# Performance work log

Hardware: AMD Instinct MI355X
Metric: run time of the kernel (lower is better)

## Reference

```python
import jax, jax.numpy as jnp
import numpy as np

B, N, C = 2, 2048, 1152
H = 16
HD = C // H  # 72
SCALE = HD ** -0.5
NEG = -100000000.0  # -1e8 bias for fp32 masked positions


def setup_inputs() -> dict:
    key = jax.random.key(0)
    k1, k2, k3, k4, k5 = jax.random.split(key, 5)
    x = jax.random.normal(k1, (B, N, C), dtype=jnp.float32)
    attn_mask = jax.random.randint(k2, (B, N), 0, 2, dtype=jnp.int32)
    w_qkv = jax.random.normal(k3, (3 * C, C), dtype=jnp.float32) * 0.02
    w_proj = jax.random.normal(k4, (C, C), dtype=jnp.float32) * 0.02
    b_proj = jax.random.normal(k5, (C,), dtype=jnp.float32) * 0.02
    return {"x": x, "attn_mask": attn_mask, "w_qkv": w_qkv, "w_proj": w_proj, "b_proj": b_proj}


def reference(x, attn_mask, w_qkv, w_proj, b_proj):
    # qkv projection: [B,N,3C] -> [3,B,H,N,HD]
    qkv = (x @ w_qkv.T).reshape(B, N, 3, H, HD).transpose(2, 0, 3, 1, 4)
    q, k, v = qkv[0], qkv[1], qkv[2]

    # additive mask bias from outer product of per-token 0/1 mask
    m = attn_mask.astype(x.dtype)          # [B,N]
    mm = m[:, :, None] * m[:, None, :]      # [B,N,N]
    bias = jnp.where(mm == 0, NEG, jnp.where(mm == 1, 0.0, mm))
    bias = bias[:, None, :, :]              # [B,1,N,N] broadcast over heads

    # math-branch attention: full QK^T, bias add, softmax, NaN patch, AV
    attn = jnp.einsum('bhqd,bhkd->bhqk', q, k) * SCALE + bias
    attn = jax.nn.softmax(attn, axis=-1)
    attn = jnp.where(jnp.isnan(attn), 0.0, attn)
    out = jnp.einsum('bhqk,bhkd->bqhd', attn, v).reshape(B, N, C)

    return out @ w_proj.T + b_proj
```

## Files before the change

kernel.cpp:

```cpp
#include <hip/hip_runtime.h>

#define B_   2
#define N_   2048
#define C_   1152
#define H_   16
#define HD_  72
#define QKV_W 3456
#define SCALE_ 0.11785113019775793f
#define NEG_  -100000000.0f
#define HDP  96
#define HDV  80
#define PRE_  0.1700219068852255f
#define FMAX_ 4.0f
#define KNEG_ 16384.0f

typedef __bf16    bf16x8 __attribute__((ext_vector_type(8)));
typedef _Float16  f16x8  __attribute__((ext_vector_type(8)));
typedef _Float16  f16x4  __attribute__((ext_vector_type(4)));
typedef float     f32x4  __attribute__((ext_vector_type(4)));

#define GLOAD_LDS16(gp, lp)                                                    \
  __builtin_amdgcn_global_load_lds(                                            \
      (const __attribute__((address_space(1))) void*)(gp),                     \
      (__attribute__((address_space(3))) void*)(lp), 16, 0, 0)

static __device__ __forceinline__ unsigned pack2h(_Float16 a, _Float16 b) {
  union { _Float16 h[2]; unsigned u; } u;
  u.h[0] = a; u.h[1] = b; return u.u;
}

__global__ __launch_bounds__(256)
void split3_f16(const float* __restrict__ x, const float* __restrict__ wq,
                const float* __restrict__ wp,
                _Float16* __restrict__ xf, _Float16* __restrict__ wqf,
                _Float16* __restrict__ wpf,
                float* __restrict__ meanAcc, int nmv,
                int n8x, int n8q, int n8p) {
  int i = blockIdx.x * 256 + threadIdx.x;
  if (i < nmv) meanAcc[i] = 0.0f;
  const float* src; _Float16* dst;
  if (i < n8x) { src = x; dst = xf; }
  else if (i < n8x + n8q) { i -= n8x; src = wq; dst = wqf; }
  else {
    i -= n8x + n8q;
    if (i >= n8p) return;
    src = wp; dst = wpf;
  }
  const float4* p = (const float4*)src + (size_t)i * 2;
  float4 a = p[0], b = p[1];
  float xs[8] = {a.x, a.y, a.z, a.w, b.x, b.y, b.z, b.w};
  f16x8 hv;
#pragma unroll
  for (int r = 0; r < 8; ++r) hv[r] = (_Float16)xs[r];
  *(f16x8*)(dst + (size_t)i * 8) = hv;
}

__global__ __launch_bounds__(256)
void gemm_f16(const _Float16* __restrict__ A, const _Float16* __restrict__ Bm,
              const float* __restrict__ bias, float* __restrict__ Cout,
              int M, int Nn, int K) {
  __shared__ uint4 lds[2][1024];

  const int tid  = threadIdx.x;
  const int wv   = tid >> 6;
  const int lane = tid & 63;
  const int wm   = wv >> 1;
  const int wn   = wv & 1;
  const int m0 = blockIdx.x * 128, n0 = blockIdx.y * 128;

  const char* gp[4];
  int gd[4];
#pragma unroll
  for (int i = 0; i < 4; ++i) {
    const int gid = wv * 4 + i;
    if (gid < 8) {
      gd[i] = gid * 64;
      gp[i] = (const char*)(A + (size_t)(m0 + gid * 16 + (lane & 15)) * K +
                            ((lane >> 4) << 3));
    } else {
      const int g2 = gid - 8;
      gd[i] = 512 + g2 * 64;
      gp[i] = (const char*)(Bm + (size_t)(n0 + g2 * 16 + (lane & 15)) * K +
                            ((lane >> 4) << 3));
    }
  }

#pragma unroll
  for (int i = 0; i < 4; ++i) {
    GLOAD_LDS16(gp[i], &lds[0][gd[i]]);
    gp[i] += 64;
  }

  f32x4 acc[4][4] = {};
  const int nk = K >> 5;

  for (int kt = 0; kt < nk; ++kt) {
    const int cur = kt & 1, nxt = cur ^ 1;
    __syncthreads();

    if (kt < nk - 1) {
#pragma unroll
      for (int i = 0; i < 4; ++i) {
        GLOAD_LDS16(gp[i], &lds[nxt][gd[i]]);
        gp[i] += 64;
      }
    }

    const uint4* cbuf = lds[cur];
    f16x8 af[4], bf[4];
#pragma unroll
    for (int t = 0; t < 4; ++t) {
      af[t] = *(const f16x8*)&cbuf[(wm * 4 + t) * 64 + lane];
      bf[t] = *(const f16x8*)&cbuf[512 + (wn * 4 + t) * 64 + lane];
    }
#pragma unroll
    for (int i = 0; i < 4; ++i)
#pragma unroll
      for (int j = 0; j < 4; ++j)
        acc[i][j] = __builtin_amdgcn_mfma_f32_16x16x32_f16(af[i], bf[j], acc[i][j], 0, 0, 0);
  }

  const int cl = lane & 15, rq = (lane >> 4) << 2;
#pragma unroll
  for (int j = 0; j < 4; ++j) {
    const int col = n0 + (wn * 4 + j) * 16 + cl;
    const float bv = bias ? bias[col] : 0.0f;
#pragma unroll
    for (int i = 0; i < 4; ++i) {
      const int row = m0 + (wm * 4 + i) * 16 + rq;
#pragma unroll
      for (int r = 0; r < 4; ++r)
        Cout[(size_t)(row + r) * Nn + col] = acc[i][j][r] + bv;
    }
  }
}

__global__ __launch_bounds__(256)
void prep_qkv(const float* __restrict__ qkv, const int* __restrict__ mask,
              _Float16* __restrict__ Qf, _Float16* __restrict__ Kf,
              _Float16* __restrict__ Vt, float* __restrict__ meanAcc) {
  const int nt = blockIdx.x, h = blockIdx.y, b = blockIdx.z;
  const int n0 = nt * 64, bh = b * H_ + h, tid = threadIdx.x;
  __shared__ float vls[64][73];

#pragma unroll
  for (int s = 0; s < 2; ++s) {
    const float* src = qkv + (size_t)(b * N_ + n0) * QKV_W + s * C_ + h * HD_;
    _Float16* of = (s == 0 ? Qf : Kf) + ((size_t)bh * N_ + n0) * HDP;
    for (int idx = tid; idx < 64 * 18; idx += 256) {
      const int row = idx / 18, c = idx % 18, d0 = c * 4;
      float4 v = *(const float4*)(src + (size_t)row * QKV_W + d0);
      if (s == 0) { v.x *= PRE_; v.y *= PRE_; v.z *= PRE_; v.w *= PRE_; }
      f16x4 hv;
      hv[0] = (_Float16)v.x; hv[1] = (_Float16)v.y;
      hv[2] = (_Float16)v.z; hv[3] = (_Float16)v.w;
      *(f16x4*)(of + (size_t)row * HDP + d0) = hv;
    }
  }

  for (int idx = tid; idx < 64 * 3; idx += 256) {
    const int row = idx / 3, c3 = idx % 3;
    const int n = n0 + row;
    f16x8 z = {};
    f16x8 qp = z, kp = z;
    if (c3 == 0) {
      qp[0] = (_Float16)1.0f;
      const int kb = (mask[b * N_ + n] != 0);
      kp[0] = (_Float16)(kb ? -FMAX_ : -KNEG_);
    }
    const size_t base = ((size_t)bh * N_ + n) * HDP + 72 + c3 * 8;
    *(f16x8*)(Qf + base) = qp;
    *(f16x8*)(Kf + base) = kp;
  }

  const float* vsrc = qkv + (size_t)(b * N_ + n0) * QKV_W + 2 * C_ + h * HD_;
  for (int idx = tid; idx < 64 * 18; idx += 256) {
    const int row = idx / 18, c = idx % 18, d0 = c * 4;
    float4 v = *(const float4*)(vsrc + (size_t)row * QKV_W + d0);
    vls[row][d0] = v.x; vls[row][d0 + 1] = v.y;
    vls[row][d0 + 2] = v.z; vls[row][d0 + 3] = v.w;
  }
  __syncthreads();
  if (tid < HD_) {
    float sum = 0.0f;
#pragma unroll 8
    for (int r = 0; r < 64; ++r) sum += vls[r][tid];
    atomicAdd(&meanAcc[bh * HD_ + tid], sum);
  }
  for (int idx = tid; idx < HDV * 64; idx += 256) {
    const int d = idx >> 6, nn = idx & 63;
    const float v = (d < HD_) ? vls[nn][d] : 0.0f;
    Vt[((size_t)bh * HDV + d) * N_ + n0 + nn] = (_Float16)v;
  }
}

__global__ __launch_bounds__(256)
void attn_mfma(const _Float16* __restrict__ Qf, const _Float16* __restrict__ Kf,
               const _Float16* __restrict__ Vt, const float* __restrict__ meanV,
               const int* __restrict__ mask, _Float16* __restrict__ att) {
  const int bh = blockIdx.x, qt = blockIdx.y;
  const int b = bh >> 4, h = bh & 15;
  const int tid = threadIdx.x, wv = tid >> 6, lane = tid & 63;
  const int lq = lane & 15;
  const int lg = lane >> 4;
  const int q0 = qt * 128;

  __shared__ uint4 lds[2][22 * 64];
  __shared__ __align__(16) _Float16 Pbuf[2][4][16][72];

  f16x8 qh[2][3];
#pragma unroll
  for (int bd = 0; bd < 2; ++bd) {
    const size_t qoff =
        ((size_t)bh * N_ + q0 + bd * 64 + wv * 16 + lq) * HDP + lg * 8;
#pragma unroll
    for (int c = 0; c < 3; ++c)
      qh[bd][c] = *(const f16x8*)(Qf + qoff + c * 32);
  }

  const _Float16* kb = Kf + (size_t)bh * N_ * HDP;
  const _Float16* vb = Vt + (size_t)bh * HDV * (size_t)N_;

  const int gstart = (wv < 2) ? wv * 6 : 12 + (wv - 2) * 5;
  const int gcount = (wv < 2) ? 6 : 5;
  const char* gptr[6];
  long gstepB[6];
  int gdst[6];
#pragma unroll
  for (int i = 0; i < 6; ++i) {
    int gid = gstart + i;
    if (gid > 21) gid = 21;
    gdst[i] = gid * 64;
    if (gid < 12) {
      const int tile = gid / 3, ch = gid - tile * 3;
      gptr[i] = (const char*)(kb + (size_t)(tile * 16 + lq) * HDP + ch * 32 + lg * 8);
      gstepB[i] = 64 * HDP * 2;
    } else {
      const int v = gid - 12, td = v >> 1, ck = v & 1;
      gptr[i] = (const char*)(vb + (size_t)(td * 16 + lq) * N_ + ck * 32 + lg * 8);
      gstepB[i] = 64 * 2;
    }
  }

#pragma unroll
  for (int i = 0; i < 6; ++i)
    if (i < gcount) {
      GLOAD_LDS16(gptr[i], &lds[0][gdst[i]]);
      gptr[i] += gstepB[i];
    }

  float l_run[2] = {0.0f, 0.0f};
  f32x4 Oacc[2][5] = {};

  for (int kt = 0; kt < N_ / 64; ++kt) {
    const int cur = kt & 1, nxt = cur ^ 1;
    __syncthreads();

    if (kt < N_ / 64 - 1) {
#pragma unroll
      for (int i = 0; i < 6; ++i)
        if (i < gcount) {
          GLOAD_LDS16(gptr[i], &lds[nxt][gdst[i]]);
          gptr[i] += gstepB[i];
        }
    }

    const uint4* cbuf = lds[cur];

    f32x4 s[2][4] = {};
#pragma unroll
    for (int ch = 0; ch < 3; ++ch)
#pragma unroll
      for (int t = 0; t < 4; ++t) {
        f16x8 kf = *(const f16x8*)&cbuf[(t * 3 + ch) * 64 + lane];
        s[0][t] = __builtin_amdgcn_mfma_f32_16x16x32_f16(kf, qh[0][ch], s[0][t], 0, 0, 0);
        s[1][t] = __builtin_amdgcn_mfma_f32_16x16x32_f16(kf, qh[1][ch], s[1][t], 0, 0, 0);
      }

#pragma unroll
    for (int bd = 0; bd < 2; ++bd) {
      float psum = 0.0f;
#pragma unroll
      for (int t = 0; t < 4; ++t) {
        const float p0 = exp2f(s[bd][t][0]);
        const float p1 = exp2f(s[bd][t][1]);
        const float p2 = exp2f(s[bd][t][2]);
        const float p3 = exp2f(s[bd][t][3]);
        psum += (p0 + p1) + (p2 + p3);
        *(uint2*)&Pbuf[bd][wv][lq][t * 16 + 4 * lg] =
            make_uint2(pack2h((_Float16)p0, (_Float16)p1),
                       pack2h((_Float16)p2, (_Float16)p3));
      }
      l_run[bd] += psum;
    }

#pragma unroll
    for (int ck = 0; ck < 2; ++ck) {
      f16x8 pf0 = *(const f16x8*)&Pbuf[0][wv][lq][ck * 32 + lg * 8];
      f16x8 pf1 = *(const f16x8*)&Pbuf[1][wv][lq][ck * 32 + lg * 8];
#pragma unroll
      for (int td = 0; td < 5; ++td) {
        f16x8 vf = *(const f16x8*)&cbuf[(12 + td * 2 + ck) * 64 + lane];
        Oacc[0][td] = __builtin_amdgcn_mfma_f32_16x16x32_f16(vf, pf0, Oacc[0][td], 0, 0, 0);
        Oacc[1][td] = __builtin_amdgcn_mfma_f32_16x16x32_f16(vf, pf1, Oacc[1][td], 0, 0, 0);
      }
    }
  }

  __syncthreads();
  float* osc = (float*)lds;
  float* myo = osc + wv * 16 * 81;
  const int rq = lane >> 2, jj = lane & 3;

#pragma unroll
  for (int bd = 0; bd < 2; ++bd) {
    float l = l_run[bd];
    l += __shfl_xor(l, 16);
    l += __shfl_xor(l, 32);
    const float inv = 1.0f / l;
#pragma unroll
    for (int td = 0; td < 5; ++td)
#pragma unroll
      for (int r = 0; r < 4; ++r)
        myo[lq * 81 + td * 16 + 4 * lg + r] = Oacc[bd][td][r] * inv;
    __syncthreads();

    const int q = q0 + bd * 64 + wv * 16 + rq;
    const int qm = (mask[b * N_ + q] != 0);
    const float* rowp = myo + rq * 81 + jj * 18;
    const float* mvp  = meanV + bh * HD_ + jj * 18;
    const size_t obase = ((size_t)(b * N_) + q) * C_ + h * HD_ + jj * 18;
#pragma unroll
    for (int e = 0; e < 9; ++e) {
      const float a = qm ? rowp[2 * e]     : mvp[2 * e]     * (1.0f / 2048.0f);
      const float c = qm ? rowp[2 * e + 1] : mvp[2 * e + 1] * (1.0f / 2048.0f);
      *(unsigned*)(att + obase + 2 * e) = pack2h((_Float16)a, (_Float16)c);
    }
    __syncthreads();
  }
}

__global__ __launch_bounds__(256)
void gemm64_nt(const float* __restrict__ A, const float* __restrict__ Bm,
               const float* __restrict__ bias, float* __restrict__ C,
               int M, int N, int K) {
  __shared__ __align__(16) float As[32][68];
  __shared__ __align__(16) float Bs[32][68];
  const int tid = threadIdx.x;
  const int tx = tid & 15, ty = tid >> 4;
  const int m0 = blockIdx.x * 64, n0 = blockIdx.y * 64;
  float acc[4][4] = {};
  for (int k0 = 0; k0 < K; k0 += 32) {
#pragma unroll
    for (int i = 0; i < 2; ++i) {
      const int idx = tid + i * 256;
      const int row = idx >> 3, kc = (idx & 7) << 2;
      float4 a = *(const float4*)(A + (size_t)(m0 + row) * K + k0 + kc);
      As[kc + 0][row] = a.x; As[kc + 1][row] = a.y;
      As[kc + 2][row] = a.z; As[kc + 3][row] = a.w;
      float4 b = *(const float4*)(Bm + (size_t)(n0 + row) * K + k0 + kc);
      Bs[kc + 0][row] = b.x; Bs[kc + 1][row] = b.y;
      Bs[kc + 2][row] = b.z; Bs[kc + 3][row] = b.w;
    }
    __syncthreads();
#pragma unroll
    for (int k = 0; k < 32; ++k) {
      float4 av4 = *(const float4*)&As[k][ty << 2];
      float4 bv4 = *(const float4*)&Bs[k][tx << 2];
      float av[4] = {av4.x, av4.y, av4.z, av4.w};
      float bv[4] = {bv4.x, bv4.y, bv4.z, bv4.w};
#pragma unroll
      for (int i = 0; i < 4; ++i)
#pragma unroll
        for (int j = 0; j < 4; ++j) acc[i][j] += av[i] * bv[j];
    }
    __syncthreads();
  }
#pragma unroll
  for (int i = 0; i < 4; ++i) {
    const int row = m0 + (ty << 2) + i, col = n0 + (tx << 2);
    float4 v = make_float4(acc[i][0], acc[i][1], acc[i][2], acc[i][3]);
    if (bias) {
      v.x += bias[col + 0]; v.y += bias[col + 1];
      v.z += bias[col + 2]; v.w += bias[col + 3];
    }
    *(float4*)(C + (size_t)row * N + col) = v;
  }
}

__global__ __launch_bounds__(256)
void attn_kernel(const float* __restrict__ qkv, const int* __restrict__ mask,
                 float* __restrict__ out) {
  const int qt = blockIdx.x, h = blockIdx.y, b = blockIdx.z;
  const int tid = threadIdx.x;
  const int q0 = qt * 64;
  __shared__ __align__(16) float qT[HD_][68];
  __shared__ __align__(16) float kT[HD_][68];
  __shared__ __align__(16) float vT[HD_][68];
  __shared__ float rowm[64], rowl[64], rowa[64];
  __shared__ float biask[64];
  __shared__ int   mq[64];
  float (*ps)[68] = (float (*)[68])kT;
  const float* qg = qkv + (size_t)(b * N_ + q0) * QKV_W + h * HD_;
  for (int idx = tid; idx < 64 * HD_; idx += 256) {
    const int qi = idx / HD_, d = idx % HD_;
    qT[d][qi] = qg[(size_t)qi * QKV_W + d];
  }
  if (tid < 64) {
    rowm[tid] = -1e30f; rowl[tid] = 0.0f;
    mq[tid] = mask[b * N_ + q0 + tid];
  }
  const int sqg = tid >> 4, skg = tid & 15;
  const int oqg = tid >> 3, ods = tid & 7;
  float o[4][9];
#pragma unroll
  for (int i = 0; i < 4; ++i)
#pragma unroll
    for (int dd = 0; dd < 9; ++dd) o[i][dd] = 0.0f;
  __syncthreads();
  for (int kt = 0; kt < N_ / 64; ++kt) {
    const int k0 = kt * 64;
    const float* kg = qkv + (size_t)(b * N_ + k0) * QKV_W + C_ + h * HD_;
    const float* vg = qkv + (size_t)(b * N_ + k0) * QKV_W + 2 * C_ + h * HD_;
    for (int idx = tid; idx < 64 * HD_; idx += 256) {
      const int kj = idx / HD_, d = idx % HD_;
      kT[d][kj] = kg[(size_t)kj * QKV_W + d];
      vT[d][kj] = vg[(size_t)kj * QKV_W + d];
    }
    if (tid < 64) biask[tid] = (mask[b * N_ + k0 + tid] != 0) ? 0.0f : NEG_;
    __syncthreads();
    float sacc[4][4] = {};
    for (int d = 0; d < HD_; ++d) {
      float4 qv4 = *(const float4*)&qT[d][sqg << 2];
      float4 kv4 = *(const float4*)&kT[d][skg << 2];
      float qa[4] = {qv4.x, qv4.y, qv4.z, qv4.w};
      float ka[4] = {kv4.x, kv4.y, kv4.z, kv4.w};
#pragma unroll
      for (int i = 0; i < 4; ++i)
#pragma unroll
        for (int j = 0; j < 4; ++j) sacc[i][j] += qa[i] * ka[j];
    }
    __syncthreads();
#pragma unroll
    for (int i = 0; i < 4; ++i) {
      const int qi = (sqg << 2) + i;
      const int qm2 = mq[qi];
#pragma unroll
      for (int j = 0; j < 4; ++j) {
        const int kj = (skg << 2) + j;
        const float bias = (qm2 != 0) ? biask[kj] : NEG_;
        ps[qi][kj] = sacc[i][j] * SCALE_ + bias;
      }
    }
    __syncthreads();
    if (tid < 64) {
      float mt = -1e30f;
#pragma unroll
      for (int j4 = 0; j4 < 16; ++j4) {
        float4 p4 = *(const float4*)&ps[tid][j4 << 2];
        mt = fmaxf(mt, fmaxf(fmaxf(p4.x, p4.y), fmaxf(p4.z, p4.w)));
      }
      const float mo = rowm[tid];
      const float nm = fmaxf(mo, mt);
      const float a = __expf(mo - nm);
      float sum = 0.0f;
#pragma unroll
      for (int j4 = 0; j4 < 16; ++j4) {
        float4 p4 = *(const float4*)&ps[tid][j4 << 2];
        p4.x = __expf(p4.x - nm); p4.y = __expf(p4.y - nm);
        p4.z = __expf(p4.z - nm); p4.w = __expf(p4.w - nm);
        sum += p4.x + p4.y + p4.z + p4.w;
        *(float4*)&ps[tid][j4 << 2] = p4;
      }
      rowl[tid] = rowl[tid] * a + sum;
      rowm[tid] = nm;
      rowa[tid] = a;
    }
    __syncthreads();
    if (tid < 128) {
#pragma unroll
      for (int i = 0; i < 4; ++i) {
        const float a = rowa[(oqg << 2) + i];
#pragma unroll
        for (int dd = 0; dd < 9; ++dd) o[i][dd] *= a;
      }
      for (int k4 = 0; k4 < 16; ++k4) {
        float4 pv4[4];
#pragma unroll
        for (int i = 0; i < 4; ++i)
          pv4[i] = *(const float4*)&ps[(oqg << 2) + i][k4 << 2];
        float pa[4][4];
#pragma unroll
        for (int i = 0; i < 4; ++i) {
          pa[i][0] = pv4[i].x; pa[i][1] = pv4[i].y;
          pa[i][2] = pv4[i].z; pa[i][3] = pv4[i].w;
        }
#pragma unroll
        for (int dd = 0; dd < 9; ++dd) {
          float4 vv4 = *(const float4*)&vT[ods * 9 + dd][k4 << 2];
          float va[4] = {vv4.x, vv4.y, vv4.z, vv4.w};
#pragma unroll
          for (int i = 0; i < 4; ++i)
            o[i][dd] += pa[i][0] * va[0] + pa[i][1] * va[1] +
                        pa[i][2] * va[2] + pa[i][3] * va[3];
        }
      }
    }
    __syncthreads();
  }
  if (tid < 128) {
#pragma unroll
    for (int i = 0; i < 4; ++i) {
      const int qi = (oqg << 2) + i;
      const float inv = 1.0f / rowl[qi];
      const size_t base = (size_t)(b * N_ + q0 + qi) * C_ + h * HD_ + ods * 9;
#pragma unroll
      for (int dd = 0; dd < 9; ++dd) out[base + dd] = o[i][dd] * inv;
    }
  }
}

extern "C" void kernel_launch(void* const* d_in, const int* in_sizes, int n_in,
                              void* d_out, int out_size, void* d_ws, size_t ws_size,
                              hipStream_t stream) {
  (void)in_sizes; (void)n_in; (void)out_size;

  const float* x      = (const float*)d_in[0];
  const int*   mask   = (const int*)  d_in[1];
  const float* w_qkv  = (const float*)d_in[2];
  const float* w_proj = (const float*)d_in[3];
  const float* b_proj = (const float*)d_in[4];
  float* out = (float*)d_out;

  const size_t XE = (size_t)B_ * N_ * C_;
  const size_t WQ = (size_t)QKV_W * C_;
  const size_t WP = (size_t)C_ * C_;
  const size_t QKVE = (size_t)B_ * N_ * QKV_W;
  const size_t QKE  = (size_t)B_ * H_ * N_ * HDP;
  const size_t VTE  = (size_t)B_ * H_ * HDV * N_;
  const int    MVN  = B_ * H_ * HD_;

  char* w = (char*)d_ws;
  float*    qkv = (float*)w;
  _Float16* att = (_Float16*)w;
  char* A0 = w + QKVE * 4;
  _Float16* x_f  = (_Float16*)A0;
  _Float16* wq_f = x_f + XE;
  _Float16* wp_f = wq_f + WQ;
  _Float16* Qf   = wp_f + WP;
  _Float16* Kf   = Qf + QKE;
  _Float16* Vt   = Kf + QKE;
  float* meanAcc = (float*)(Vt + VTE);
  const size_t need = (size_t)((char*)(meanAcc + MVN) - w);

  if (ws_size >= need) {
    const int n8x = (int)(XE / 8), n8q = (int)(WQ / 8), n8p = (int)(WP / 8);
    const int nblk = (n8x + n8q + n8p + 255) / 256;
    split3_f16<<<nblk, 256, 0, stream>>>(x, w_qkv, w_proj, x_f, wq_f, wp_f,
                                         meanAcc, MVN, n8x, n8q, n8p);

    gemm_f16<<<dim3(32, 27), 256, 0, stream>>>(x_f, wq_f, nullptr, qkv,
                                               B_ * N_, QKV_W, C_);
    prep_qkv<<<dim3(32, 16, 2), 256, 0, stream>>>(qkv, mask, Qf, Kf, Vt, meanAcc);

    attn_mfma<<<dim3(32, 16), 256, 0, stream>>>(Qf, Kf, Vt, meanAcc, mask, att);

    gemm_f16<<<dim3(32, 9), 256, 0, stream>>>(att, wp_f, b_proj, out,
                                              B_ * N_, C_, C_);
  } else {
    float* qkv_f = (float*)d_ws;
    float* att_f = qkv_f + QKVE;
    gemm64_nt<<<dim3(64, 54), 256, 0, stream>>>(x, w_qkv, nullptr, qkv_f,
                                                B_ * N_, QKV_W, C_);
    attn_kernel<<<dim3(32, 16, 2), 256, 0, stream>>>(qkv_f, mask, att_f);
    gemm64_nt<<<dim3(64, 18), 256, 0, stream>>>(att_f, w_proj, b_proj, out,
                                                B_ * N_, C_, C_);
  }
}
```

Baseline: 298.2 us.

## Fuse QKV layout prep into QKV GEMM epilogue, drop fp32 intermediate

Removes the prep_qkv kernel and the fp32 QKV intermediate buffer. The QKV GEMM epilogue now writes Q (pre-scaled), K, and transposed V directly in fp16, and accumulates per-head V column sums via shuffles and atomics. The padding columns and mask entries are written by the conversion kernel instead. This saves a kernel launch and an fp32 round trip through global memory. The cost is scattered 2-byte stores in the Q/K epilogue.

Result: faster. 281.3 us (-5.7%).

```diff
diff --git a/kernel.cpp b/kernel.cpp
--- a/kernel.cpp
+++ b/kernel.cpp
@@ -14,7 +14,6 @@
 #define FMAX_ 4.0f
 #define KNEG_ 16384.0f
 
-typedef __bf16    bf16x8 __attribute__((ext_vector_type(8)));
 typedef _Float16  f16x8  __attribute__((ext_vector_type(8)));
 typedef _Float16  f16x4  __attribute__((ext_vector_type(4)));
 typedef float     f32x4  __attribute__((ext_vector_type(4)));
@@ -34,18 +33,50 @@
                 const float* __restrict__ wp,
                 _Float16* __restrict__ xf, _Float16* __restrict__ wqf,
                 _Float16* __restrict__ wpf,
+                _Float16* __restrict__ Qf, _Float16* __restrict__ Kf,
+                _Float16* __restrict__ Vt, const int* __restrict__ mask,
                 float* __restrict__ meanAcc, int nmv,
                 int n8x, int n8q, int n8p) {
   int i = blockIdx.x * 256 + threadIdx.x;
   if (i < nmv) meanAcc[i] = 0.0f;
-  const float* src; _Float16* dst;
+
+  const float* src = nullptr; _Float16* dst = nullptr;
   if (i < n8x) { src = x; dst = xf; }
-  else if (i < n8x + n8q) { i -= n8x; src = wq; dst = wqf; }
   else {
-    i -= n8x + n8q;
-    if (i >= n8p) return;
-    src = wp; dst = wpf;
-  }
+    i -= n8x;
+    if (i < n8q) { src = wq; dst = wqf; }
+    else {
+      i -= n8q;
+      if (i < n8p) { src = wp; dst = wpf; }
+      else {
+        i -= n8p;
+        if (i < 32 * 2048 * 3) {
+          const int bh = i / (2048 * 3);
+          int rem = i - bh * (2048 * 3);
+          const int n = rem / 3, c3 = rem - (rem / 3) * 3;
+          f16x8 qp = {}, kp = {};
+          if (c3 == 0) {
+            qp[0] = (_Float16)1.0f;
+            const int kb = (mask[(bh >> 4) * N_ + n] != 0);
+            kp[0] = (_Float16)(kb ? -FMAX_ : -KNEG_);
+          }
+          const size_t base = ((size_t)bh * N_ + n) * HDP + 72 + c3 * 8;
+          *(f16x8*)(Qf + base) = qp;
+          *(f16x8*)(Kf + base) = kp;
+          return;
+        }
+        i -= 32 * 2048 * 3;
+        if (i < 32 * 8 * 256) {
+          const int bh = i >> 11, rem = i & 2047;
+          const int dp = rem >> 8, nc = rem & 255;
+          f16x8 z = {};
+          *(f16x8*)(Vt + ((size_t)bh * HDV + 72 + dp) * N_ + nc * 8) = z;
+        }
+        return;
+      }
+    }
+  }
+
   const float4* p = (const float4*)src + (size_t)i * 2;
   float4 a = p[0], b = p[1];
   float xs[8] = {a.x, a.y, a.z, a.w, b.x, b.y, b.z, b.w};
@@ -136,61 +167,116 @@
 }
 
 __global__ __launch_bounds__(256)
-void prep_qkv(const float* __restrict__ qkv, const int* __restrict__ mask,
-              _Float16* __restrict__ Qf, _Float16* __restrict__ Kf,
-              _Float16* __restrict__ Vt, float* __restrict__ meanAcc) {
-  const int nt = blockIdx.x, h = blockIdx.y, b = blockIdx.z;
-  const int n0 = nt * 64, bh = b * H_ + h, tid = threadIdx.x;
-  __shared__ float vls[64][73];
-
-#pragma unroll
-  for (int s = 0; s < 2; ++s) {
-    const float* src = qkv + (size_t)(b * N_ + n0) * QKV_W + s * C_ + h * HD_;
-    _Float16* of = (s == 0 ? Qf : Kf) + ((size_t)bh * N_ + n0) * HDP;
-    for (int idx = tid; idx < 64 * 18; idx += 256) {
-      const int row = idx / 18, c = idx % 18, d0 = c * 4;
-      float4 v = *(const float4*)(src + (size_t)row * QKV_W + d0);
-      if (s == 0) { v.x *= PRE_; v.y *= PRE_; v.z *= PRE_; v.w *= PRE_; }
-      f16x4 hv;
-      hv[0] = (_Float16)v.x; hv[1] = (_Float16)v.y;
-      hv[2] = (_Float16)v.z; hv[3] = (_Float16)v.w;
-      *(f16x4*)(of + (size_t)row * HDP + d0) = hv;
-    }
-  }
-
-  for (int idx = tid; idx < 64 * 3; idx += 256) {
-    const int row = idx / 3, c3 = idx % 3;
-    const int n = n0 + row;
-    f16x8 z = {};
-    f16x8 qp = z, kp = z;
-    if (c3 == 0) {
-      qp[0] = (_Float16)1.0f;
-      const int kb = (mask[b * N_ + n] != 0);
-      kp[0] = (_Float16)(kb ? -FMAX_ : -KNEG_);
-    }
-    const size_t base = ((size_t)bh * N_ + n) * HDP + 72 + c3 * 8;
-    *(f16x8*)(Qf + base) = qp;
-    *(f16x8*)(Kf + base) = kp;
-  }
-
-  const float* vsrc = qkv + (size_t)(b * N_ + n0) * QKV_W + 2 * C_ + h * HD_;
-  for (int idx = tid; idx < 64 * 18; idx += 256) {
-    const int row = idx / 18, c = idx % 18, d0 = c * 4;
-    float4 v = *(const float4*)(vsrc + (size_t)row * QKV_W + d0);
-    vls[row][d0] = v.x; vls[row][d0 + 1] = v.y;
-    vls[row][d0 + 2] = v.z; vls[row][d0 + 3] = v.w;
-  }
-  __syncthreads();
-  if (tid < HD_) {
-    float sum = 0.0f;
-#pragma unroll 8
-    for (int r = 0; r < 64; ++r) sum += vls[r][tid];
-    atomicAdd(&meanAcc[bh * HD_ + tid], sum);
-  }
-  for (int idx = tid; idx < HDV * 64; idx += 256) {
-    const int d = idx >> 6, nn = idx & 63;
-    const float v = (d < HD_) ? vls[nn][d] : 0.0f;
-    Vt[((size_t)bh * HDV + d) * N_ + n0 + nn] = (_Float16)v;
+void gemm_qkv_fused(const _Float16* __restrict__ A, const _Float16* __restrict__ Bm,
+                    _Float16* __restrict__ Qf, _Float16* __restrict__ Kf,
+                    _Float16* __restrict__ Vt, float* __restrict__ meanAcc) {
+  __shared__ uint4 lds[2][1024];
+
+  const int K = C_;
+  const int tid  = threadIdx.x;
+  const int wv   = tid >> 6;
+  const int lane = tid & 63;
+  const int wm   = wv >> 1;
+  const int wn   = wv & 1;
+  const int m0 = blockIdx.x * 128, n0 = blockIdx.y * 128;
+
+  const char* gp[4];
+  int gd[4];
+#pragma unroll
+  for (int i = 0; i < 4; ++i) {
+    const int gid = wv * 4 + i;
+    if (gid < 8) {
+      gd[i] = gid * 64;
+      gp[i] = (const char*)(A + (size_t)(m0 + gid * 16 + (lane & 15)) * K +
+                            ((lane >> 4) << 3));
+    } else {
+      const int g2 = gid - 8;
+      gd[i] = 512 + g2 * 64;
+      gp[i] = (const char*)(Bm + (size_t)(n0 + g2 * 16 + (lane & 15)) * K +
+                            ((lane >> 4) << 3));
+    }
+  }
+
+#pragma unroll
+  for (int i = 0; i < 4; ++i) {
+    GLOAD_LDS16(gp[i], &lds[0][gd[i]]);
+    gp[i] += 64;
+  }
+
+  f32x4 acc[4][4] = {};
+  const int nk = K >> 5;
+
+  for (int kt = 0; kt < nk; ++kt) {
+    const int cur = kt & 1, nxt = cur ^ 1;
+    __syncthreads();
+
+    if (kt < nk - 1) {
+#pragma unroll
+      for (int i = 0; i < 4; ++i) {
+        GLOAD_LDS16(gp[i], &lds[nxt][gd[i]]);
+        gp[i] += 64;
+      }
+    }
+
+    const uint4* cbuf = lds[cur];
+    f16x8 af[4], bf[4];
+#pragma unroll
+    for (int t = 0; t < 4; ++t) {
+      af[t] = *(const f16x8*)&cbuf[(wm * 4 + t) * 64 + lane];
+      bf[t] = *(const f16x8*)&cbuf[512 + (wn * 4 + t) * 64 + lane];
+    }
+#pragma unroll
+    for (int i = 0; i < 4; ++i)
+#pragma unroll
+      for (int j = 0; j < 4; ++j)
+        acc[i][j] = __builtin_amdgcn_mfma_f32_16x16x32_f16(af[i], bf[j], acc[i][j], 0, 0, 0);
+  }
+
+  const int s = n0 / C_;
+  const int b = m0 >> 11;
+  const int nloc = m0 & 2047;
+  const int cl = lane & 15, rq = (lane >> 4) << 2;
+
+  if (s < 2) {
+    _Float16* dst = (s == 0) ? Qf : Kf;
+    const float sc = (s == 0) ? PRE_ : 1.0f;
+#pragma unroll
+    for (int j = 0; j < 4; ++j) {
+      const int col  = n0 + (wn * 4 + j) * 16 + cl;
+      const int dseg = col - s * C_;
+      const int h = dseg / HD_, hd = dseg - h * HD_;
+      _Float16* base =
+          dst + ((size_t)(b * H_ + h) * N_ + nloc + wm * 64) * HDP + hd;
+#pragma unroll
+      for (int i = 0; i < 4; ++i) {
+        const int r0 = i * 16 + rq;
+#pragma unroll
+        for (int r = 0; r < 4; ++r)
+          base[(size_t)(r0 + r) * HDP] = (_Float16)(acc[i][j][r] * sc);
+      }
+    }
+  } else {
+#pragma unroll
+    for (int j = 0; j < 4; ++j) {
+      const int col = n0 + (wn * 4 + j) * 16 + cl;
+      const int dv  = col - 2 * C_;
+      const int h = dv / HD_, hd = dv - h * HD_;
+      const int bh = b * H_ + h;
+      _Float16* base = Vt + ((size_t)bh * HDV + hd) * N_ + nloc + wm * 64;
+      float colsum = 0.0f;
+#pragma unroll
+      for (int i = 0; i < 4; ++i) {
+        const int r0 = i * 16 + rq;
+        *(uint2*)(base + r0) =
+            make_uint2(pack2h((_Float16)acc[i][j][0], (_Float16)acc[i][j][1]),
+                       pack2h((_Float16)acc[i][j][2], (_Float16)acc[i][j][3]));
+        colsum += (acc[i][j][0] + acc[i][j][1]) + (acc[i][j][2] + acc[i][j][3]);
+      }
+      colsum += __shfl_xor(colsum, 16);
+      colsum += __shfl_xor(colsum, 32);
+      if ((lane >> 4) == 0)
+        atomicAdd(&meanAcc[bh * HD_ + hd], colsum);
+    }
   }
 }
 
@@ -541,10 +627,8 @@
   const int    MVN  = B_ * H_ * HD_;
 
   char* w = (char*)d_ws;
-  float*    qkv = (float*)w;
-  _Float16* att = (_Float16*)w;
-  char* A0 = w + QKVE * 4;
-  _Float16* x_f  = (_Float16*)A0;
+  _Float16* att  = (_Float16*)w;
+  _Float16* x_f  = att + XE;
   _Float16* wq_f = x_f + XE;
   _Float16* wp_f = wq_f + WQ;
   _Float16* Qf   = wp_f + WP;
@@ -555,13 +639,15 @@
 
   if (ws_size >= need) {
     const int n8x = (int)(XE / 8), n8q = (int)(WQ / 8), n8p = (int)(WP / 8);
-    const int nblk = (n8x + n8q + n8p + 255) / 256;
-    split3_f16<<<nblk, 256, 0, stream>>>(x, w_qkv, w_proj, x_f, wq_f, wp_f,
-                                         meanAcc, MVN, n8x, n8q, n8p);
-
-    gemm_f16<<<dim3(32, 27), 256, 0, stream>>>(x_f, wq_f, nullptr, qkv,
-                                               B_ * N_, QKV_W, C_);
-    prep_qkv<<<dim3(32, 16, 2), 256, 0, stream>>>(qkv, mask, Qf, Kf, Vt, meanAcc);
+    const int npadQK = 32 * 2048 * 3;
+    const int npadV  = 32 * 8 * 256;
+    const int total  = n8x + n8q + n8p + npadQK + npadV;
+    split3_f16<<<(total + 255) / 256, 256, 0, stream>>>(
+        x, w_qkv, w_proj, x_f, wq_f, wp_f, Qf, Kf, Vt, mask,
+        meanAcc, MVN, n8x, n8q, n8p);
+
+    gemm_qkv_fused<<<dim3(32, 27), 256, 0, stream>>>(x_f, wq_f, Qf, Kf, Vt,
+                                                     meanAcc);
 
     attn_mfma<<<dim3(32, 16), 256, 0, stream>>>(Qf, Kf, Vt, meanAcc, mask, att);
 
```
